# Kernel tuning notes

Hardware: AMD Instinct MI355X
Metric: run time of the kernel (lower is better)

The kernel has to match this reference:

```python
import jax, jax.numpy as jnp
import numpy as np

N = 64        # n_nodes per graph
H = 128       # hidden channels (128x0e + 128x1o)
NB = 8        # radial bessel basis size
L = 2         # num_interactions
R_MAX = 5.0
AVG_NEIGH = 63.0
DIM = 3       # output vector dim
B = 64        # batch (vmapped)
T = 32        # time-embedding dim
S = 5         # num_species


def _edges(n):
    # fully-connected graph, no self loops (static shapes, jit-friendly)
    s, r = np.meshgrid(np.arange(n), np.arange(n), indexing='ij')
    m = s != r
    return jnp.asarray(s[m]), jnp.asarray(r[m])


def setup_inputs() -> dict:
    key = jax.random.key(0)
    ks = jax.random.split(key, 12)
    sc = 0.05
    return {
        'positions': jax.random.normal(ks[0], (B, N, 3), jnp.float32),
        'node_features': jax.random.randint(ks[1], (B, N), 0, S).astype(jnp.int64),
        'global_features': jax.random.normal(ks[2], (B, T), jnp.float32),
        'emb': jax.random.normal(ks[3], (S, H), jnp.float32) * sc,
        'Wt': jax.random.normal(ks[4], (T, H), jnp.float32) * sc,
        'Wr1': jax.random.normal(ks[5], (L, NB, H), jnp.float32) * sc,
        'Wr2': jax.random.normal(ks[6], (L, H, H), jnp.float32) * sc,
        'Wupd': jax.random.normal(ks[7], (L, H, H), jnp.float32) * sc,
        'Wmix': jax.random.normal(ks[8], (L, H, H), jnp.float32) * sc,
        'Wg1': jax.random.normal(ks[9], (H, H), jnp.float32) * sc,
        'Wg2': jax.random.normal(ks[10], (H, H), jnp.float32) * sc,
        'final_scaling': jnp.ones((), jnp.float32),
    }


def _call_single(pos, z, t, emb, Wt, Wr1, Wr2, Wupd, Wmix, Wg1, Wg2, final_scaling):
    snd, rcv = _edges(N)
    ev = pos[rcv] - pos[snd]                               # [E,3] edge vectors (gather)
    r = jnp.sqrt(jnp.sum(ev * ev, axis=-1) + 1e-12)        # [E]
    u = ev / r[:, None]                                    # unit directions
    # Bessel radial basis with cosine cutoff (r_max acts as soft radius graph)
    n = jnp.arange(1, NB + 1, dtype=pos.dtype)
    rb = jnp.sin(n * jnp.pi * r[:, None] / R_MAX) / r[:, None]   # [E,NB]
    fc = 0.5 * (jnp.cos(jnp.pi * r / R_MAX) + 1.0) * (r < R_MAX)
    rb = rb * fc[:, None]
    # node embedding from species + time embedding
    h = emb[z] + t @ Wt                                    # [N,H] scalar features
    v = jnp.zeros((N, H, DIM), pos.dtype)                  # vector (1o) features
    for l in range(L):
        w = jax.nn.silu(rb @ Wr1[l]) @ Wr2[l]              # [E,H] radial weights
        m0 = w * h[snd]                                    # [E,H] scalar messages
        m1 = m0[:, :, None] * u[:, None, :]                # [E,H,3] vector messages
        a0 = jax.ops.segment_sum(m0, rcv, num_segments=N) / AVG_NEIGH
        a1 = jax.ops.segment_sum(m1, rcv, num_segments=N) / AVG_NEIGH
        h = h + a0 @ Wupd[l]
        v = v + jnp.einsum('ngd,gh->nhd', a1, Wmix[l])
    # equivariant readout: scalar gate per channel contracts vector channels
    g = jax.nn.silu(h @ Wg1) @ Wg2                         # [N,H]
    out = jnp.einsum('nhd,nh->nd', v, g)                   # [N,3]
    return out * final_scaling


def reference(positions, node_features, global_features, emb, Wt, Wr1, Wr2, Wupd, Wmix, Wg1, Wg2, final_scaling):
    f = lambda p, z, t: _call_single(p, z, t, emb, Wt, Wr1, Wr2, Wupd, Wmix, Wg1, Wg2, final_scaling)
    return jax.vmap(f)(positions, node_features, global_features)
```

## Files before the change

### kernel.cpp

```cpp
#include <hip/hip_runtime.h>
#include <math.h>

#define NN 64
#define HH 128
#define NBB 8
#define TT 32
#define BB 64
#define NROW (BB * NN)
#define PLANE ((size_t)NROW * HH)
#define WR1OFF (8 * 16384)

typedef __attribute__((ext_vector_type(8))) short short8;
typedef __attribute__((ext_vector_type(4))) float f32x4;
typedef __attribute__((ext_vector_type(2))) unsigned int u32x2;

__device__ __forceinline__ float silu_f(float x) {
  return x * __builtin_amdgcn_rcpf(1.0f + __expf(-x));
}

__device__ __forceinline__ unsigned short bf1(float x) {
  __bf16 h = (__bf16)x;
  return *(unsigned short*)&h;
}
__device__ __forceinline__ unsigned bf2(float lo, float hi) {
  return (unsigned)bf1(lo) | ((unsigned)bf1(hi) << 16);
}

__device__ __forceinline__ void gemm8(
    const unsigned short (*sA)[136], const unsigned short* __restrict__ Bp,
    int w, int nlo, int quad, f32x4 C[2]) {
  const short8 z8 = {0, 0, 0, 0, 0, 0, 0, 0};
  short8 afr[4];
#pragma unroll
  for (int kt = 0; kt < 4; ++kt)
    afr[kt] = (nlo < 8) ? *(const short8*)&sA[nlo][kt * 32 + quad * 8] : z8;
#pragma unroll
  for (int nt = 0; nt < 2; ++nt)
#pragma unroll
    for (int kt = 0; kt < 4; ++kt) {
      short8 bfr = *(const short8*)&Bp[((kt * 128 + w * 32 + nt * 16 + nlo) * 4 + quad) * 8];
      C[nt] = __builtin_amdgcn_mfma_f32_16x16x32_bf16(afr[kt], bfr, C[nt], 0, 0, 0);
    }
}

__global__ __launch_bounds__(256) void k_init(
    const float* __restrict__ emb, const int* __restrict__ z,
    const float* __restrict__ gf, const float* __restrict__ Wt,
    const float* __restrict__ Wr1, const float* __restrict__ Wr2,
    const float* __restrict__ Wupd, const float* __restrict__ Wmix,
    const float* __restrict__ Wg1, const float* __restrict__ Wg2,
    float* __restrict__ h, unsigned short* __restrict__ Wpack) {
  __shared__ float tvec[HH];
  __shared__ int sz[NN];
  int b4 = blockIdx.x, tid = threadIdx.x;
  {
    int p2 = b4 * 256 + tid;
    int p = p2 * 2;
    int m = p >> 14;
    int j = p & 7;
    int q = (p >> 3) & 3;
    int n = (p >> 5) & 127;
    int kt = (p >> 12) & 3;
    int k = kt * 32 + q * 8 + j;
    const float* src;
    int base;
    if (m < 2) { src = Wr2; base = m * 16384; }
    else if (m < 4) { src = Wupd; base = (m - 2) * 16384; }
    else if (m < 6) { src = Wmix; base = (m - 4) * 16384; }
    else if (m == 6) { src = Wg1; base = 0; }
    else { src = Wg2; base = 0; }
    float v0 = src[base + k * 128 + n];
    float v1 = src[base + (k + 1) * 128 + n];
    *(unsigned*)&Wpack[p] = bf2(v0, v1);
  }
  if (tid < 32) {
    int e = b4 * 32 + tid;
    int l = e >> 12, p = e & 4095;
    int n = p >> 5, q = (p >> 3) & 3, j = p & 7;
    float val = (q == 0) ? Wr1[l * NBB * HH + j * HH + n] : 0.f;
    Wpack[WR1OFF + l * 4096 + p] = bf1(val);
  }
  if (b4 < 64) {
    int b = b4;
    if (tid < NN) sz[tid] = z[b * NN + tid];
    if (tid < HH) {
      float acc = 0.f;
#pragma unroll
      for (int k = 0; k < TT; ++k) acc += gf[b * TT + k] * Wt[k * HH + tid];
      tvec[tid] = acc;
    }
    __syncthreads();
    for (int i = tid; i < NN * HH; i += 256) {
      int n = i >> 7, c = i & 127;
      h[(size_t)b * NN * HH + i] = emb[sz[n] * HH + c] + tvec[c];
    }
  }
}

__global__ __launch_bounds__(256) void k_layer0(
    const float* __restrict__ pos, const float* __restrict__ hA,
    unsigned short* __restrict__ apout, const unsigned short* __restrict__ Wpack) {
  __shared__ __align__(16) unsigned short sh_S[NN][136];
  __shared__ __align__(16) unsigned short sh_M0T[4][32][72];
  __shared__ __align__(16) unsigned short sh_rbh[2][NN][8];
  __shared__ __align__(16) unsigned short sh_ub[2][4][NN];

  int blk = blockIdx.x;
  int b = blk >> 4, rp4 = blk & 15;
  int r0 = rp4 * 4;
  int tid = threadIdx.x;
  int w = tid >> 6, lane = tid & 63;
  int nlo = lane & 15, quad = lane >> 4;

  f32x4 hbv[4][2];
#pragma unroll
  for (int mt = 0; mt < 4; ++mt)
#pragma unroll
    for (int nt = 0; nt < 2; ++nt)
#pragma unroll
      for (int reg = 0; reg < 4; ++reg)
        hbv[mt][nt][reg] =
            hA[((size_t)b * NN + mt * 16 + quad * 4 + reg) * HH + w * 32 + nt * 16 + nlo];

  const unsigned short* Wr1p = Wpack + WR1OFF;
  short8 bw[2];
#pragma unroll
  for (int nt = 0; nt < 2; ++nt)
    bw[nt] = *(const short8*)&Wr1p[((w * 32 + nt * 16 + nlo) * 4 + quad) * 8];
  const unsigned short* Bbase = Wpack;
  short8 bfr[4][2];
#pragma unroll
  for (int kt = 0; kt < 4; ++kt)
#pragma unroll
    for (int nt = 0; nt < 2; ++nt)
      bfr[kt][nt] = *(const short8*)&Bbase[((kt * 128 + w * 32 + nt * 16 + nlo) * 4 + quad) * 8];

  const short8 zero8 = {0, 0, 0, 0, 0, 0, 0, 0};

#pragma unroll
  for (int pp = 0; pp < 2; ++pp) {
    int rb0 = r0 + pp * 2;
    {
      int s = tid & 63;
      int ksel = (tid >> 6) & 1;
      int ri = (tid >> 7) & 1;
      int r = rb0 + ri;
      const float* pb = pos + b * NN * 3;
      float dx = pb[r * 3 + 0] - pb[s * 3 + 0];
      float dy = pb[r * 3 + 1] - pb[s * 3 + 1];
      float dz = pb[r * 3 + 2] - pb[s * 3 + 2];
      float rr = sqrtf(dx * dx + dy * dy + dz * dz + 1e-12f);
      float inv = __builtin_amdgcn_rcpf(rr);
      const float invAvg = 1.0f / 63.0f;
      if (ksel == 0) {
        float ia = inv * invAvg;
        sh_ub[ri][1][s] = bf1(dx * ia);
        sh_ub[ri][2][s] = bf1(dy * ia);
        sh_ub[ri][3][s] = bf1(dz * ia);
      } else {
        sh_ub[ri][0][s] = bf1(invAvg);
      }
      const float PI_OVER_5 = 0.628318530717958647692f;
      float fc = (s != r && rr < 5.0f) ? 0.5f * (__cosf(PI_OVER_5 * rr) + 1.0f) : 0.0f;
      float base = PI_OVER_5 * rr;
      float sc = inv * fc;
      int k0 = ksel * 4;
      float v0 = __sinf((float)(k0 + 1) * base) * sc;
      float v1 = __sinf((float)(k0 + 2) * base) * sc;
      float v2 = __sinf((float)(k0 + 3) * base) * sc;
      float v3 = __sinf((float)(k0 + 4) * base) * sc;
      *(unsigned*)&sh_rbh[ri][s][k0]     = bf2(v0, v1);
      *(unsigned*)&sh_rbh[ri][s][k0 + 2] = bf2(v2, v3);
    }
    __syncthreads();

    short8 au[2][2];
#pragma unroll
    for (int ri = 0; ri < 2; ++ri)
#pragma unroll
      for (int kt = 0; kt < 2; ++kt)
        au[ri][kt] = (nlo < 4) ? *(const short8*)&sh_ub[ri][nlo][kt * 32 + quad * 8] : zero8;

#pragma unroll
    for (int ri = 0; ri < 2; ++ri) {
#pragma unroll
      for (int mtp = 0; mtp < 2; ++mtp) {
        f32x4 Cs[2][2];
#pragma unroll
        for (int mi = 0; mi < 2; ++mi)
#pragma unroll
          for (int nt = 0; nt < 2; ++nt) Cs[mi][nt] = (f32x4){0.f, 0.f, 0.f, 0.f};
#pragma unroll
        for (int mi = 0; mi < 2; ++mi) {
          int mt = mtp * 2 + mi;
          short8 afr = (quad == 0) ? *(const short8*)&sh_rbh[ri][mt * 16 + nlo][0] : zero8;
#pragma unroll
          for (int nt = 0; nt < 2; ++nt)
            Cs[mi][nt] = __builtin_amdgcn_mfma_f32_16x16x32_bf16(afr, bw[nt], Cs[mi][nt], 0, 0, 0);
        }
#pragma unroll
        for (int mi = 0; mi < 2; ++mi)
#pragma unroll
          for (int nt = 0; nt < 2; ++nt)
#pragma unroll
            for (int reg = 0; reg < 4; ++reg) {
              int s = (mtp * 2 + mi) * 16 + quad * 4 + reg;
              int c = w * 32 + nt * 16 + nlo;
              sh_S[s][c] = bf1(silu_f(Cs[mi][nt][reg]));
            }
      }
      __syncthreads();

#pragma unroll
      for (int mt = 0; mt < 4; ++mt) {
        short8 afr[4];
        int s_a = mt * 16 + nlo;
#pragma unroll
        for (int kt = 0; kt < 4; ++kt)
          afr[kt] = *(const short8*)&sh_S[s_a][kt * 32 + quad * 8];
#pragma unroll
        for (int nt = 0; nt < 2; ++nt) {
          f32x4 C = {0.f, 0.f, 0.f, 0.f};
#pragma unroll
          for (int kt = 0; kt < 4; ++kt)
            C = __builtin_amdgcn_mfma_f32_16x16x32_bf16(afr[kt], bfr[kt][nt], C, 0, 0, 0);
          f32x4 m0 = C * hbv[mt][nt];
          u32x2 pk;
          pk.x = bf2(m0[0], m0[1]);
          pk.y = bf2(m0[2], m0[3]);
          *(u32x2*)&sh_M0T[w][nt * 16 + nlo][mt * 16 + quad * 4] = pk;
        }
      }
      {
        f32x4 Cu[2] = {{0, 0, 0, 0}, {0, 0, 0, 0}};
#pragma unroll
        for (int nt = 0; nt < 2; ++nt)
#pragma unroll
          for (int kt = 0; kt < 2; ++kt) {
            short8 bm = *(const short8*)&sh_M0T[w][nt * 16 + nlo][kt * 32 + quad * 8];
            Cu[nt] = __builtin_amdgcn_mfma_f32_16x16x32_bf16(au[ri][kt], bm, Cu[nt], 0, 0, 0);
          }
        if (quad == 0) {
#pragma unroll
          for (int nt = 0; nt < 2; ++nt) {
            size_t base = (size_t)(b * NN + rb0 + ri) * HH + w * 32 + nt * 16 + nlo;
#pragma unroll
            for (int reg = 0; reg < 4; ++reg)
              apout[reg * PLANE + base] = bf1(Cu[nt][reg]);
          }
        }
      }
      if (!(pp == 1 && ri == 1)) __syncthreads();
    }
  }
}

__global__ __launch_bounds__(256) void k_fused(
    const float* __restrict__ pos, const float* __restrict__ hA,
    unsigned short* __restrict__ apbf, const unsigned short* __restrict__ Wpack,
    const float* __restrict__ fs, float* __restrict__ out) {
  __shared__ __align__(16) unsigned char smem[38912];
  unsigned short (*sh_S)[136]      = (unsigned short (*)[136])smem;
  unsigned short (*sh_M0T)[32][72] = (unsigned short (*)[32][72])(smem + 17408);
  unsigned short (*sh_rbh)[NN][8]  = (unsigned short (*)[NN][8])(smem + 35840);
  unsigned short (*sh_ub)[4][NN]   = (unsigned short (*)[4][NN])(smem + 37888);

  int blk = blockIdx.x;
  int b = blk >> 3, u8 = blk & 7;
  int tid = threadIdx.x;
  int w = tid >> 6, lane = tid & 63;
  int nlo = lane & 15, quad = lane >> 4;
  const short8 zero8 = {0, 0, 0, 0, 0, 0, 0, 0};

  f32x4 hbv[4][2];
#pragma unroll
  for (int mt = 0; mt < 4; ++mt)
#pragma unroll
    for (int nt = 0; nt < 2; ++nt)
#pragma unroll
      for (int reg = 0; reg < 4; ++reg)
        hbv[mt][nt][reg] =
            hA[((size_t)b * NN + mt * 16 + quad * 4 + reg) * HH + w * 32 + nt * 16 + nlo];

  for (int i = tid; i < NN * 64; i += 256) {
    int s = i >> 6, c2 = (i & 63) * 2;
    *(unsigned*)&sh_S[s][c2] =
        *(const unsigned*)&apbf[((size_t)b * NN + s) * HH + c2];
  }
  __syncthreads();
  {
    const unsigned short* Bu = Wpack + 2 * 16384;
#pragma unroll
    for (int mt = 0; mt < 4; ++mt) {
      short8 afr[4];
#pragma unroll
      for (int kt = 0; kt < 4; ++kt)
        afr[kt] = *(const short8*)&sh_S[mt * 16 + nlo][kt * 32 + quad * 8];
#pragma unroll
      for (int nt = 0; nt < 2; ++nt)
#pragma unroll
        for (int kt = 0; kt < 4; ++kt) {
          short8 bfr2 = *(const short8*)&Bu[((kt * 128 + w * 32 + nt * 16 + nlo) * 4 + quad) * 8];
          hbv[mt][nt] = __builtin_amdgcn_mfma_f32_16x16x32_bf16(afr[kt], bfr2, hbv[mt][nt], 0, 0, 0);
        }
    }
  }
  __syncthreads();

  const unsigned short* Wr1p = Wpack + WR1OFF + 4096;
  short8 bw[2];
#pragma unroll
  for (int nt = 0; nt < 2; ++nt)
    bw[nt] = *(const short8*)&Wr1p[((w * 32 + nt * 16 + nlo) * 4 + quad) * 8];
  const unsigned short* Bbase = Wpack + 16384;
  short8 bfr[4][2];
#pragma unroll
  for (int kt = 0; kt < 4; ++kt)
#pragma unroll
    for (int nt = 0; nt < 2; ++nt)
      bfr[kt][nt] = *(const short8*)&Bbase[((kt * 128 + w * 32 + nt * 16 + nlo) * 4 + quad) * 8];

  for (int unit = 0; unit < 2; ++unit) {
    int r0 = (u8 * 2 + unit) * 4;
#pragma unroll
    for (int pp = 0; pp < 2; ++pp) {
      int rb0 = r0 + pp * 2;
      {
        int s = tid & 63;
        int ksel = (tid >> 6) & 1;
        int ri = (tid >> 7) & 1;
        int r = rb0 + ri;
        const float* pb = pos + b * NN * 3;
        float dx = pb[r * 3 + 0] - pb[s * 3 + 0];
        float dy = pb[r * 3 + 1] - pb[s * 3 + 1];
        float dz = pb[r * 3 + 2] - pb[s * 3 + 2];
        float rr = sqrtf(dx * dx + dy * dy + dz * dz + 1e-12f);
        float inv = __builtin_amdgcn_rcpf(rr);
        const float invAvg = 1.0f / 63.0f;
        if (ksel == 0) {
          float ia = inv * invAvg;
          sh_ub[ri][1][s] = bf1(dx * ia);
          sh_ub[ri][2][s] = bf1(dy * ia);
          sh_ub[ri][3][s] = bf1(dz * ia);
        } else {
          sh_ub[ri][0][s] = bf1(invAvg);
        }
        const float PI_OVER_5 = 0.628318530717958647692f;
        float fc = (s != r && rr < 5.0f) ? 0.5f * (__cosf(PI_OVER_5 * rr) + 1.0f) : 0.0f;
        float base = PI_OVER_5 * rr;
        float sc = inv * fc;
        int k0 = ksel * 4;
        float v0 = __sinf((float)(k0 + 1) * base) * sc;
        float v1 = __sinf((float)(k0 + 2) * base) * sc;
        float v2 = __sinf((float)(k0 + 3) * base) * sc;
        float v3 = __sinf((float)(k0 + 4) * base) * sc;
        *(unsigned*)&sh_rbh[ri][s][k0]     = bf2(v0, v1);
        *(unsigned*)&sh_rbh[ri][s][k0 + 2] = bf2(v2, v3);
      }
      __syncthreads();

      short8 au[2][2];
#pragma unroll
      for (int ri = 0; ri < 2; ++ri)
#pragma unroll
        for (int kt = 0; kt < 2; ++kt)
          au[ri][kt] = (nlo < 4) ? *(const short8*)&sh_ub[ri][nlo][kt * 32 + quad * 8] : zero8;

#pragma unroll
      for (int ri = 0; ri < 2; ++ri) {
#pragma unroll
        for (int mtp = 0; mtp < 2; ++mtp) {
          f32x4 Cs[2][2];
#pragma unroll
          for (int mi = 0; mi < 2; ++mi)
#pragma unroll
            for (int nt = 0; nt < 2; ++nt) Cs[mi][nt] = (f32x4){0.f, 0.f, 0.f, 0.f};
#pragma unroll
          for (int mi = 0; mi < 2; ++mi) {
            int mt = mtp * 2 + mi;
            short8 afr = (quad == 0) ? *(const short8*)&sh_rbh[ri][mt * 16 + nlo][0] : zero8;
#pragma unroll
            for (int nt = 0; nt < 2; ++nt)
              Cs[mi][nt] = __builtin_amdgcn_mfma_f32_16x16x32_bf16(afr, bw[nt], Cs[mi][nt], 0, 0, 0);
          }
#pragma unroll
          for (int mi = 0; mi < 2; ++mi)
#pragma unroll
            for (int nt = 0; nt < 2; ++nt)
#pragma unroll
              for (int reg = 0; reg < 4; ++reg) {
                int s = (mtp * 2 + mi) * 16 + quad * 4 + reg;
                int c = w * 32 + nt * 16 + nlo;
                sh_S[s][c] = bf1(silu_f(Cs[mi][nt][reg]));
              }
        }
        __syncthreads();

#pragma unroll
        for (int mt = 0; mt < 4; ++mt) {
          short8 afr[4];
          int s_a = mt * 16 + nlo;
#pragma unroll
          for (int kt = 0; kt < 4; ++kt)
            afr[kt] = *(const short8*)&sh_S[s_a][kt * 32 + quad * 8];
#pragma unroll
          for (int nt = 0; nt < 2; ++nt) {
            f32x4 C = {0.f, 0.f, 0.f, 0.f};
#pragma unroll
            for (int kt = 0; kt < 4; ++kt)
              C = __builtin_amdgcn_mfma_f32_16x16x32_bf16(afr[kt], bfr[kt][nt], C, 0, 0, 0);
            f32x4 m0 = C * hbv[mt][nt];
            u32x2 pk;
            pk.x = bf2(m0[0], m0[1]);
            pk.y = bf2(m0[2], m0[3]);
            *(u32x2*)&sh_M0T[w][nt * 16 + nlo][mt * 16 + quad * 4] = pk;
          }
        }
        {
          f32x4 Cu[2] = {{0, 0, 0, 0}, {0, 0, 0, 0}};
#pragma unroll
          for (int nt = 0; nt < 2; ++nt)
#pragma unroll
            for (int kt = 0; kt < 2; ++kt) {
              short8 bm = *(const short8*)&sh_M0T[w][nt * 16 + nlo][kt * 32 + quad * 8];
              Cu[nt] = __builtin_amdgcn_mfma_f32_16x16x32_bf16(au[ri][kt], bm, Cu[nt], 0, 0, 0);
            }
          if (quad == 0) {
#pragma unroll
            for (int nt = 0; nt < 2; ++nt) {
              size_t base = (size_t)(b * NN + rb0 + ri) * HH + w * 32 + nt * 16 + nlo;
#pragma unroll
              for (int reg = 0; reg < 4; ++reg)
                apbf[(4 + reg) * PLANE + base] = bf1(Cu[nt][reg]);
            }
          }
        }
        __syncthreads();
      }
    }
  }

  {
    unsigned short (*sh_a)[8][136] = (unsigned short (*)[8][136])smem;
    unsigned short (*sh_h)[136]    = (unsigned short (*)[136])(smem + 17408);
    float (*red)[8][3]             = (float (*)[8][3])(smem + 17408 + 2176);
    int row0 = blk * 8;
    for (int i = tid; i < 8 * 8 * 64; i += 256) {
      int p = i >> 9, rr = (i >> 6) & 7, c2 = (i & 63) * 2;
      *(unsigned*)&sh_a[p][rr][c2] =
          *(const unsigned*)&apbf[p * PLANE + (size_t)(row0 + rr) * HH + c2];
    }
    f32x4 Ch[2];
#pragma unroll
    for (int nt = 0; nt < 2; ++nt)
#pragma unroll
      for (int reg = 0; reg < 4; ++reg)
        Ch[nt][reg] = (quad < 2)
            ? hA[(size_t)(row0 + quad * 4 + reg) * HH + w * 32 + nt * 16 + nlo] : 0.f;
    __syncthreads();
    gemm8(sh_a[0], Wpack + 2 * 16384, w, nlo, quad, Ch);
    gemm8(sh_a[4], Wpack + 3 * 16384, w, nlo, quad, Ch);
    f32x4 Cx[2] = {{0,0,0,0},{0,0,0,0}};
    f32x4 Cy[2] = {{0,0,0,0},{0,0,0,0}};
    f32x4 Cz[2] = {{0,0,0,0},{0,0,0,0}};
    gemm8(sh_a[1], Wpack + 4 * 16384, w, nlo, quad, Cx);
    gemm8(sh_a[5], Wpack + 5 * 16384, w, nlo, quad, Cx);
    gemm8(sh_a[2], Wpack + 4 * 16384, w, nlo, quad, Cy);
    gemm8(sh_a[6], Wpack + 5 * 16384, w, nlo, quad, Cy);
    gemm8(sh_a[3], Wpack + 4 * 16384, w, nlo, quad, Cz);
    gemm8(sh_a[7], Wpack + 5 * 16384, w, nlo, quad, Cz);
    if (quad < 2) {
#pragma unroll
      for (int nt = 0; nt < 2; ++nt)
#pragma unroll
        for (int reg = 0; reg < 4; ++reg)
          sh_h[quad * 4 + reg][w * 32 + nt * 16 + nlo] = bf1(Ch[nt][reg]);
    }
    __syncthreads();
    unsigned short (*sh_q)[136] = sh_a[0];
    f32x4 Cq[2] = {{0,0,0,0},{0,0,0,0}};
    gemm8(sh_h, Wpack + 6 * 16384, w, nlo, quad, Cq);
    if (quad < 2) {
#pragma unroll
      for (int nt = 0; nt < 2; ++nt)
#pragma unroll
        for (int reg = 0; reg < 4; ++reg)
          sh_q[quad * 4 + reg][w * 32 + nt * 16 + nlo] = bf1(silu_f(Cq[nt][reg]));
    }
    __syncthreads();
    f32x4 Cg[2] = {{0,0,0,0},{0,0,0,0}};
    gemm8(sh_q, Wpack + 7 * 16384, w, nlo, quad, Cg);
    float pr[3][4];
#pragma unroll
    for (int d = 0; d < 3; ++d)
#pragma unroll
      for (int reg = 0; reg < 4; ++reg) pr[d][reg] = 0.f;
#pragma unroll
    for (int nt = 0; nt < 2; ++nt)
#pragma unroll
      for (int reg = 0; reg < 4; ++reg) {
        float gv = Cg[nt][reg];
        pr[0][reg] += gv * Cx[nt][reg];
        pr[1][reg] += gv * Cy[nt][reg];
        pr[2][reg] += gv * Cz[nt][reg];
      }
#pragma unroll
    for (int off = 1; off < 16; off <<= 1)
#pragma unroll
      for (int d = 0; d < 3; ++d)
#pragma unroll
        for (int reg = 0; reg < 4; ++reg)
          pr[d][reg] += __shfl_xor(pr[d][reg], off);
    if (nlo == 0 && quad < 2) {
#pragma unroll
      for (int d = 0; d < 3; ++d)
#pragma unroll
        for (int reg = 0; reg < 4; ++reg)
          red[w][quad * 4 + reg][d] = pr[d][reg];
    }
    __syncthreads();
    if (tid < 24) {
      int row = tid / 3, d = tid % 3;
      float s = red[0][row][d] + red[1][row][d] + red[2][row][d] + red[3][row][d];
      out[(size_t)(row0 + row) * 3 + d] = s * fs[0];
    }
  }
}

extern "C" void kernel_launch(void* const* d_in, const int* in_sizes, int n_in,
                              void* d_out, int out_size, void* d_ws, size_t ws_size,
                              hipStream_t stream) {
  const float* pos  = (const float*)d_in[0];
  const int*   z    = (const int*)d_in[1];
  const float* gf   = (const float*)d_in[2];
  const float* emb  = (const float*)d_in[3];
  const float* Wt   = (const float*)d_in[4];
  const float* Wr1  = (const float*)d_in[5];
  const float* Wr2  = (const float*)d_in[6];
  const float* Wupd = (const float*)d_in[7];
  const float* Wmix = (const float*)d_in[8];
  const float* Wg1  = (const float*)d_in[9];
  const float* Wg2  = (const float*)d_in[10];
  const float* fs   = (const float*)d_in[11];
  float* out = (float*)d_out;

  float* ws = (float*)d_ws;
  float* hA = ws;
  unsigned short* apbf = (unsigned short*)(ws + PLANE);
  unsigned short* Wpack = (unsigned short*)(ws + 5 * PLANE);

  k_init<<<dim3(256), dim3(256), 0, stream>>>(emb, z, gf, Wt, Wr1, Wr2, Wupd,
                                              Wmix, Wg1, Wg2, hA, Wpack);
  k_layer0<<<dim3(BB * 16), dim3(256), 0, stream>>>(pos, hA, apbf, Wpack);
  k_fused<<<dim3(512), dim3(256), 0, stream>>>(pos, hA, apbf, Wpack, fs, out);
}
```

Measured before the change: 141.3 us.

## Keep layer-1 aggregates in LDS and compute edge features for four receivers at once

The fused kernel now writes the layer-1 aggregated messages (planes 4-7) directly into a shared-memory buffer that the readout stage reads, instead of storing them to global memory and reading them back. Both layer kernels also compute edge geometry for all four receivers in one pass, which halves the barrier-separated prep phases. This removes a global round trip and some synchronisation. In exchange, LDS use per block grows (about 50 KB in the fused kernel), which may reduce occupancy.

```diff
diff --git a/kernel.cpp b/kernel.cpp
--- a/kernel.cpp
+++ b/kernel.cpp
@@ -102,8 +102,8 @@
     unsigned short* __restrict__ apout, const unsigned short* __restrict__ Wpack) {
   __shared__ __align__(16) unsigned short sh_S[NN][136];
   __shared__ __align__(16) unsigned short sh_M0T[4][32][72];
-  __shared__ __align__(16) unsigned short sh_rbh[2][NN][8];
-  __shared__ __align__(16) unsigned short sh_ub[2][4][NN];
+  __shared__ __align__(16) unsigned short sh_rbh[4][NN][8];
+  __shared__ __align__(16) unsigned short sh_ub[4][4][NN];
 
   int blk = blockIdx.x;
   int b = blk >> 4, rp4 = blk & 15;
@@ -111,6 +111,7 @@
   int tid = threadIdx.x;
   int w = tid >> 6, lane = tid & 63;
   int nlo = lane & 15, quad = lane >> 4;
+  const short8 zero8 = {0, 0, 0, 0, 0, 0, 0, 0};
 
   f32x4 hbv[4][2];
 #pragma unroll
@@ -135,16 +136,188 @@
     for (int nt = 0; nt < 2; ++nt)
       bfr[kt][nt] = *(const short8*)&Bbase[((kt * 128 + w * 32 + nt * 16 + nlo) * 4 + quad) * 8];
 
+  {
+    int s = tid & 63;
+    int ri4 = tid >> 6;
+    int r = r0 + ri4;
+    const float* pb = pos + b * NN * 3;
+    float dx = pb[r * 3 + 0] - pb[s * 3 + 0];
+    float dy = pb[r * 3 + 1] - pb[s * 3 + 1];
+    float dz = pb[r * 3 + 2] - pb[s * 3 + 2];
+    float rr = sqrtf(dx * dx + dy * dy + dz * dz + 1e-12f);
+    float inv = __builtin_amdgcn_rcpf(rr);
+    const float invAvg = 1.0f / 63.0f;
+    float ia = inv * invAvg;
+    sh_ub[ri4][0][s] = bf1(invAvg);
+    sh_ub[ri4][1][s] = bf1(dx * ia);
+    sh_ub[ri4][2][s] = bf1(dy * ia);
+    sh_ub[ri4][3][s] = bf1(dz * ia);
+    const float PI_OVER_5 = 0.628318530717958647692f;
+    float fc = (s != r && rr < 5.0f) ? 0.5f * (__cosf(PI_OVER_5 * rr) + 1.0f) : 0.0f;
+    float base = PI_OVER_5 * rr;
+    float sc = inv * fc;
+#pragma unroll
+    for (int k0 = 0; k0 < 8; k0 += 4) {
+      float v0 = __sinf((float)(k0 + 1) * base) * sc;
+      float v1 = __sinf((float)(k0 + 2) * base) * sc;
+      float v2 = __sinf((float)(k0 + 3) * base) * sc;
+      float v3 = __sinf((float)(k0 + 4) * base) * sc;
+      *(unsigned*)&sh_rbh[ri4][s][k0]     = bf2(v0, v1);
+      *(unsigned*)&sh_rbh[ri4][s][k0 + 2] = bf2(v2, v3);
+    }
+  }
+  __syncthreads();
+
+#pragma unroll
+  for (int rsel = 0; rsel < 4; ++rsel) {
+#pragma unroll
+    for (int mtp = 0; mtp < 2; ++mtp) {
+      f32x4 Cs[2][2];
+#pragma unroll
+      for (int mi = 0; mi < 2; ++mi)
+#pragma unroll
+        for (int nt = 0; nt < 2; ++nt) Cs[mi][nt] = (f32x4){0.f, 0.f, 0.f, 0.f};
+#pragma unroll
+      for (int mi = 0; mi < 2; ++mi) {
+        int mt = mtp * 2 + mi;
+        short8 afr = (quad == 0) ? *(const short8*)&sh_rbh[rsel][mt * 16 + nlo][0] : zero8;
+#pragma unroll
+        for (int nt = 0; nt < 2; ++nt)
+          Cs[mi][nt] = __builtin_amdgcn_mfma_f32_16x16x32_bf16(afr, bw[nt], Cs[mi][nt], 0, 0, 0);
+      }
+#pragma unroll
+      for (int mi = 0; mi < 2; ++mi)
+#pragma unroll
+        for (int nt = 0; nt < 2; ++nt)
+#pragma unroll
+          for (int reg = 0; reg < 4; ++reg) {
+            int s = (mtp * 2 + mi) * 16 + quad * 4 + reg;
+            int c = w * 32 + nt * 16 + nlo;
+            sh_S[s][c] = bf1(silu_f(Cs[mi][nt][reg]));
+          }
+    }
+    __syncthreads();
+
+#pragma unroll
+    for (int mt = 0; mt < 4; ++mt) {
+      short8 afr[4];
+      int s_a = mt * 16 + nlo;
+#pragma unroll
+      for (int kt = 0; kt < 4; ++kt)
+        afr[kt] = *(const short8*)&sh_S[s_a][kt * 32 + quad * 8];
+#pragma unroll
+      for (int nt = 0; nt < 2; ++nt) {
+        f32x4 C = {0.f, 0.f, 0.f, 0.f};
+#pragma unroll
+        for (int kt = 0; kt < 4; ++kt)
+          C = __builtin_amdgcn_mfma_f32_16x16x32_bf16(afr[kt], bfr[kt][nt], C, 0, 0, 0);
+        f32x4 m0 = C * hbv[mt][nt];
+        u32x2 pk;
+        pk.x = bf2(m0[0], m0[1]);
+        pk.y = bf2(m0[2], m0[3]);
+        *(u32x2*)&sh_M0T[w][nt * 16 + nlo][mt * 16 + quad * 4] = pk;
+      }
+    }
+    {
+      short8 au[2];
+#pragma unroll
+      for (int kt = 0; kt < 2; ++kt)
+        au[kt] = (nlo < 4) ? *(const short8*)&sh_ub[rsel][nlo][kt * 32 + quad * 8] : zero8;
+      f32x4 Cu[2] = {{0, 0, 0, 0}, {0, 0, 0, 0}};
+#pragma unroll
+      for (int nt = 0; nt < 2; ++nt)
+#pragma unroll
+        for (int kt = 0; kt < 2; ++kt) {
+          short8 bm = *(const short8*)&sh_M0T[w][nt * 16 + nlo][kt * 32 + quad * 8];
+          Cu[nt] = __builtin_amdgcn_mfma_f32_16x16x32_bf16(au[kt], bm, Cu[nt], 0, 0, 0);
+        }
+      if (quad == 0) {
+#pragma unroll
+        for (int nt = 0; nt < 2; ++nt) {
+          size_t base = (size_t)(b * NN + r0 + rsel) * HH + w * 32 + nt * 16 + nlo;
+#pragma unroll
+          for (int reg = 0; reg < 4; ++reg)
+            apout[reg * PLANE + base] = bf1(Cu[nt][reg]);
+        }
+      }
+    }
+    if (rsel != 3) __syncthreads();
+  }
+}
+
+__global__ __launch_bounds__(256) void k_fused(
+    const float* __restrict__ pos, const float* __restrict__ hA,
+    unsigned short* __restrict__ apbf, const unsigned short* __restrict__ Wpack,
+    const float* __restrict__ fs, float* __restrict__ out) {
+  __shared__ __align__(16) unsigned char smem[50688];
+  unsigned short (*sh_S)[136]      = (unsigned short (*)[136])smem;
+  unsigned short (*sh_M0T)[32][72] = (unsigned short (*)[32][72])(smem + 17408);
+  unsigned short (*sh_rbh)[NN][8]  = (unsigned short (*)[NN][8])(smem + 35840);
+  unsigned short (*sh_ub)[4][NN]   = (unsigned short (*)[4][NN])(smem + 39936);
+  unsigned short (*sh_a47)[8][136] = (unsigned short (*)[8][136])(smem + 41984);
+
+  int blk = blockIdx.x;
+  int b = blk >> 3, u8 = blk & 7;
+  int tid = threadIdx.x;
+  int w = tid >> 6, lane = tid & 63;
+  int nlo = lane & 15, quad = lane >> 4;
   const short8 zero8 = {0, 0, 0, 0, 0, 0, 0, 0};
 
-#pragma unroll
-  for (int pp = 0; pp < 2; ++pp) {
-    int rb0 = r0 + pp * 2;
+  f32x4 hbv[4][2];
+#pragma unroll
+  for (int mt = 0; mt < 4; ++mt)
+#pragma unroll
+    for (int nt = 0; nt < 2; ++nt)
+#pragma unroll
+      for (int reg = 0; reg < 4; ++reg)
+        hbv[mt][nt][reg] =
+            hA[((size_t)b * NN + mt * 16 + quad * 4 + reg) * HH + w * 32 + nt * 16 + nlo];
+
+  for (int i = tid; i < NN * 64; i += 256) {
+    int s = i >> 6, c2 = (i & 63) * 2;
+    *(unsigned*)&sh_S[s][c2] =
+        *(const unsigned*)&apbf[((size_t)b * NN + s) * HH + c2];
+  }
+  __syncthreads();
+  {
+    const unsigned short* Bu = Wpack + 2 * 16384;
+#pragma unroll
+    for (int mt = 0; mt < 4; ++mt) {
+      short8 afr[4];
+#pragma unroll
+      for (int kt = 0; kt < 4; ++kt)
+        afr[kt] = *(const short8*)&sh_S[mt * 16 + nlo][kt * 32 + quad * 8];
+#pragma unroll
+      for (int nt = 0; nt < 2; ++nt)
+#pragma unroll
+        for (int kt = 0; kt < 4; ++kt) {
+          short8 bfr2 = *(const short8*)&Bu[((kt * 128 + w * 32 + nt * 16 + nlo) * 4 + quad) * 8];
+          hbv[mt][nt] = __builtin_amdgcn_mfma_f32_16x16x32_bf16(afr[kt], bfr2, hbv[mt][nt], 0, 0, 0);
+        }
+    }
+  }
+  __syncthreads();
+
+  const unsigned short* Wr1p = Wpack + WR1OFF + 4096;
+  short8 bw[2];
+#pragma unroll
+  for (int nt = 0; nt < 2; ++nt)
+    bw[nt] = *(const short8*)&Wr1p[((w * 32 + nt * 16 + nlo) * 4 + quad) * 8];
+  const unsigned short* Bbase = Wpack + 16384;
+  short8 bfr[4][2];
+#pragma unroll
+  for (int kt = 0; kt < 4; ++kt)
+#pragma unroll
+    for (int nt = 0; nt < 2; ++nt)
+      bfr[kt][nt] = *(const short8*)&Bbase[((kt * 128 + w * 32 + nt * 16 + nlo) * 4 + quad) * 8];
+
+  for (int unit = 0; unit < 2; ++unit) {
+    int r0 = u8 * 8 + unit * 4;
+
     {
       int s = tid & 63;
-      int ksel = (tid >> 6) & 1;
-      int ri = (tid >> 7) & 1;
-      int r = rb0 + ri;
+      int ri4 = tid >> 6;
+      int r = r0 + ri4;
       const float* pb = pos + b * NN * 3;
       float dx = pb[r * 3 + 0] - pb[s * 3 + 0];
       float dy = pb[r * 3 + 1] - pb[s * 3 + 1];
@@ -152,37 +325,30 @@
       float rr = sqrtf(dx * dx + dy * dy + dz * dz + 1e-12f);
       float inv = __builtin_amdgcn_rcpf(rr);
       const float invAvg = 1.0f / 63.0f;
-      if (ksel == 0) {
-        float ia = inv * invAvg;
-        sh_ub[ri][1][s] = bf1(dx * ia);
-        sh_ub[ri][2][s] = bf1(dy * ia);
-        sh_ub[ri][3][s] = bf1(dz * ia);
-      } else {
-        sh_ub[ri][0][s] = bf1(invAvg);
-      }
+      float ia = inv * invAvg;
+      sh_ub[ri4][0][s] = bf1(invAvg);
+      sh_ub[ri4][1][s] = bf1(dx * ia);
+      sh_ub[ri4][2][s] = bf1(dy * ia);
+      sh_ub[ri4][3][s] = bf1(dz * ia);
       const float PI_OVER_5 = 0.628318530717958647692f;
       float fc = (s != r && rr < 5.0f) ? 0.5f * (__cosf(PI_OVER_5 * rr) + 1.0f) : 0.0f;
       float base = PI_OVER_5 * rr;
       float sc = inv * fc;
-      int k0 = ksel * 4;
-      float v0 = __sinf((float)(k0 + 1) * base) * sc;
-      float v1 = __sinf((float)(k0 + 2) * base) * sc;
-      float v2 = __sinf((float)(k0 + 3) * base) * sc;
-      float v3 = __sinf((float)(k0 + 4) * base) * sc;
-      *(unsigned*)&sh_rbh[ri][s][k0]     = bf2(v0, v1);
-      *(unsigned*)&sh_rbh[ri][s][k0 + 2] = bf2(v2, v3);
-    }
-    __syncthreads();
-
-    short8 au[2][2];
-#pragma unroll
-    for (int ri = 0; ri < 2; ++ri)
-#pragma unroll
-      for (int kt = 0; kt < 2; ++kt)
-        au[ri][kt] = (nlo < 4) ? *(const short8*)&sh_ub[ri][nlo][kt * 32 + quad * 8] : zero8;
-
-#pragma unroll
-    for (int ri = 0; ri < 2; ++ri) {
+#pragma unroll
+      for (int k0 = 0; k0 < 8; k0 += 4) {
+        float v0 = __sinf((float)(k0 + 1) * base) * sc;
+        float v1 = __sinf((float)(k0 + 2) * base) * sc;
+        float v2 = __sinf((float)(k0 + 3) * base) * sc;
+        float v3 = __sinf((float)(k0 + 4) * base) * sc;
+        *(unsigned*)&sh_rbh[ri4][s][k0]     = bf2(v0, v1);
+        *(unsigned*)&sh_rbh[ri4][s][k0 + 2] = bf2(v2, v3);
+      }
+    }
+    __syncthreads();
+
+#pragma unroll
+    for (int rsel = 0; rsel < 4; ++rsel) {
+      int lr = unit * 4 + rsel;
 #pragma unroll
       for (int mtp = 0; mtp < 2; ++mtp) {
         f32x4 Cs[2][2];
@@ -193,7 +359,7 @@
 #pragma unroll
         for (int mi = 0; mi < 2; ++mi) {
           int mt = mtp * 2 + mi;
-          short8 afr = (quad == 0) ? *(const short8*)&sh_rbh[ri][mt * 16 + nlo][0] : zero8;
+          short8 afr = (quad == 0) ? *(const short8*)&sh_rbh[rsel][mt * 16 + nlo][0] : zero8;
 #pragma unroll
           for (int nt = 0; nt < 2; ++nt)
             Cs[mi][nt] = __builtin_amdgcn_mfma_f32_16x16x32_bf16(afr, bw[nt], Cs[mi][nt], 0, 0, 0);
@@ -232,222 +398,40 @@
         }
       }
       {
+        short8 au[2];
+#pragma unroll
+        for (int kt = 0; kt < 2; ++kt)
+          au[kt] = (nlo < 4) ? *(const short8*)&sh_ub[rsel][nlo][kt * 32 + quad * 8] : zero8;
         f32x4 Cu[2] = {{0, 0, 0, 0}, {0, 0, 0, 0}};
 #pragma unroll
         for (int nt = 0; nt < 2; ++nt)
 #pragma unroll
           for (int kt = 0; kt < 2; ++kt) {
             short8 bm = *(const short8*)&sh_M0T[w][nt * 16 + nlo][kt * 32 + quad * 8];
-            Cu[nt] = __builtin_amdgcn_mfma_f32_16x16x32_bf16(au[ri][kt], bm, Cu[nt], 0, 0, 0);
+            Cu[nt] = __builtin_amdgcn_mfma_f32_16x16x32_bf16(au[kt], bm, Cu[nt], 0, 0, 0);
           }
         if (quad == 0) {
 #pragma unroll
           for (int nt = 0; nt < 2; ++nt) {
-            size_t base = (size_t)(b * NN + rb0 + ri) * HH + w * 32 + nt * 16 + nlo;
+            int c = w * 32 + nt * 16 + nlo;
 #pragma unroll
             for (int reg = 0; reg < 4; ++reg)
-              apout[reg * PLANE + base] = bf1(Cu[nt][reg]);
+              sh_a47[reg][lr][c] = bf1(Cu[nt][reg]);
           }
         }
       }
-      if (!(pp == 1 && ri == 1)) __syncthreads();
-    }
-  }
-}
-
-__global__ __launch_bounds__(256) void k_fused(
-    const float* __restrict__ pos, const float* __restrict__ hA,
-    unsigned short* __restrict__ apbf, const unsigned short* __restrict__ Wpack,
-    const float* __restrict__ fs, float* __restrict__ out) {
-  __shared__ __align__(16) unsigned char smem[38912];
-  unsigned short (*sh_S)[136]      = (unsigned short (*)[136])smem;
-  unsigned short (*sh_M0T)[32][72] = (unsigned short (*)[32][72])(smem + 17408);
-  unsigned short (*sh_rbh)[NN][8]  = (unsigned short (*)[NN][8])(smem + 35840);
-  unsigned short (*sh_ub)[4][NN]   = (unsigned short (*)[4][NN])(smem + 37888);
-
-  int blk = blockIdx.x;
-  int b = blk >> 3, u8 = blk & 7;
-  int tid = threadIdx.x;
-  int w = tid >> 6, lane = tid & 63;
-  int nlo = lane & 15, quad = lane >> 4;
-  const short8 zero8 = {0, 0, 0, 0, 0, 0, 0, 0};
-
-  f32x4 hbv[4][2];
-#pragma unroll
-  for (int mt = 0; mt < 4; ++mt)
-#pragma unroll
-    for (int nt = 0; nt < 2; ++nt)
-#pragma unroll
-      for (int reg = 0; reg < 4; ++reg)
-        hbv[mt][nt][reg] =
-            hA[((size_t)b * NN + mt * 16 + quad * 4 + reg) * HH + w * 32 + nt * 16 + nlo];
-
-  for (int i = tid; i < NN * 64; i += 256) {
-    int s = i >> 6, c2 = (i & 63) * 2;
-    *(unsigned*)&sh_S[s][c2] =
-        *(const unsigned*)&apbf[((size_t)b * NN + s) * HH + c2];
-  }
-  __syncthreads();
+      __syncthreads();
+    }
+  }
+
   {
-    const unsigned short* Bu = Wpack + 2 * 16384;
-#pragma unroll
-    for (int mt = 0; mt < 4; ++mt) {
-      short8 afr[4];
-#pragma unroll
-      for (int kt = 0; kt < 4; ++kt)
-        afr[kt] = *(const short8*)&sh_S[mt * 16 + nlo][kt * 32 + quad * 8];
-#pragma unroll
-      for (int nt = 0; nt < 2; ++nt)
-#pragma unroll
-        for (int kt = 0; kt < 4; ++kt) {
-          short8 bfr2 = *(const short8*)&Bu[((kt * 128 + w * 32 + nt * 16 + nlo) * 4 + quad) * 8];
-          hbv[mt][nt] = __builtin_amdgcn_mfma_f32_16x16x32_bf16(afr[kt], bfr2, hbv[mt][nt], 0, 0, 0);
-        }
-    }
-  }
-  __syncthreads();
-
-  const unsigned short* Wr1p = Wpack + WR1OFF + 4096;
-  short8 bw[2];
-#pragma unroll
-  for (int nt = 0; nt < 2; ++nt)
-    bw[nt] = *(const short8*)&Wr1p[((w * 32 + nt * 16 + nlo) * 4 + quad) * 8];
-  const unsigned short* Bbase = Wpack + 16384;
-  short8 bfr[4][2];
-#pragma unroll
-  for (int kt = 0; kt < 4; ++kt)
-#pragma unroll
-    for (int nt = 0; nt < 2; ++nt)
-      bfr[kt][nt] = *(const short8*)&Bbase[((kt * 128 + w * 32 + nt * 16 + nlo) * 4 + quad) * 8];
-
-  for (int unit = 0; unit < 2; ++unit) {
-    int r0 = (u8 * 2 + unit) * 4;
-#pragma unroll
-    for (int pp = 0; pp < 2; ++pp) {
-      int rb0 = r0 + pp * 2;
-      {
-        int s = tid & 63;
-        int ksel = (tid >> 6) & 1;
-        int ri = (tid >> 7) & 1;
-        int r = rb0 + ri;
-        const float* pb = pos + b * NN * 3;
-        float dx = pb[r * 3 + 0] - pb[s * 3 + 0];
-        float dy = pb[r * 3 + 1] - pb[s * 3 + 1];
-        float dz = pb[r * 3 + 2] - pb[s * 3 + 2];
-        float rr = sqrtf(dx * dx + dy * dy + dz * dz + 1e-12f);
-        float inv = __builtin_amdgcn_rcpf(rr);
-        const float invAvg = 1.0f / 63.0f;
-        if (ksel == 0) {
-          float ia = inv * invAvg;
-          sh_ub[ri][1][s] = bf1(dx * ia);
-          sh_ub[ri][2][s] = bf1(dy * ia);
-          sh_ub[ri][3][s] = bf1(dz * ia);
-        } else {
-          sh_ub[ri][0][s] = bf1(invAvg);
-        }
-        const float PI_OVER_5 = 0.628318530717958647692f;
-        float fc = (s != r && rr < 5.0f) ? 0.5f * (__cosf(PI_OVER_5 * rr) + 1.0f) : 0.0f;
-        float base = PI_OVER_5 * rr;
-        float sc = inv * fc;
-        int k0 = ksel * 4;
-        float v0 = __sinf((float)(k0 + 1) * base) * sc;
-        float v1 = __sinf((float)(k0 + 2) * base) * sc;
-        float v2 = __sinf((float)(k0 + 3) * base) * sc;
-        float v3 = __sinf((float)(k0 + 4) * base) * sc;
-        *(unsigned*)&sh_rbh[ri][s][k0]     = bf2(v0, v1);
-        *(unsigned*)&sh_rbh[ri][s][k0 + 2] = bf2(v2, v3);
-      }
-      __syncthreads();
-
-      short8 au[2][2];
-#pragma unroll
-      for (int ri = 0; ri < 2; ++ri)
-#pragma unroll
-        for (int kt = 0; kt < 2; ++kt)
-          au[ri][kt] = (nlo < 4) ? *(const short8*)&sh_ub[ri][nlo][kt * 32 + quad * 8] : zero8;
-
-#pragma unroll
-      for (int ri = 0; ri < 2; ++ri) {
-#pragma unroll
-        for (int mtp = 0; mtp < 2; ++mtp) {
-          f32x4 Cs[2][2];
-#pragma unroll
-          for (int mi = 0; mi < 2; ++mi)
-#pragma unroll
-            for (int nt = 0; nt < 2; ++nt) Cs[mi][nt] = (f32x4){0.f, 0.f, 0.f, 0.f};
-#pragma unroll
-          for (int mi = 0; mi < 2; ++mi) {
-            int mt = mtp * 2 + mi;
-            short8 afr = (quad == 0) ? *(const short8*)&sh_rbh[ri][mt * 16 + nlo][0] : zero8;
-#pragma unroll
-            for (int nt = 0; nt < 2; ++nt)
-              Cs[mi][nt] = __builtin_amdgcn_mfma_f32_16x16x32_bf16(afr, bw[nt], Cs[mi][nt], 0, 0, 0);
-          }
-#pragma unroll
-          for (int mi = 0; mi < 2; ++mi)
-#pragma unroll
-            for (int nt = 0; nt < 2; ++nt)
-#pragma unroll
-              for (int reg = 0; reg < 4; ++reg) {
-                int s = (mtp * 2 + mi) * 16 + quad * 4 + reg;
-                int c = w * 32 + nt * 16 + nlo;
-                sh_S[s][c] = bf1(silu_f(Cs[mi][nt][reg]));
-              }
-        }
-        __syncthreads();
-
-#pragma unroll
-        for (int mt = 0; mt < 4; ++mt) {
-          short8 afr[4];
-          int s_a = mt * 16 + nlo;
-#pragma unroll
-          for (int kt = 0; kt < 4; ++kt)
-            afr[kt] = *(const short8*)&sh_S[s_a][kt * 32 + quad * 8];
-#pragma unroll
-          for (int nt = 0; nt < 2; ++nt) {
-            f32x4 C = {0.f, 0.f, 0.f, 0.f};
-#pragma unroll
-            for (int kt = 0; kt < 4; ++kt)
-              C = __builtin_amdgcn_mfma_f32_16x16x32_bf16(afr[kt], bfr[kt][nt], C, 0, 0, 0);
-            f32x4 m0 = C * hbv[mt][nt];
-            u32x2 pk;
-            pk.x = bf2(m0[0], m0[1]);
-            pk.y = bf2(m0[2], m0[3]);
-            *(u32x2*)&sh_M0T[w][nt * 16 + nlo][mt * 16 + quad * 4] = pk;
-          }
-        }
-        {
-          f32x4 Cu[2] = {{0, 0, 0, 0}, {0, 0, 0, 0}};
-#pragma unroll
-          for (int nt = 0; nt < 2; ++nt)
-#pragma unroll
-            for (int kt = 0; kt < 2; ++kt) {
-              short8 bm = *(const short8*)&sh_M0T[w][nt * 16 + nlo][kt * 32 + quad * 8];
-              Cu[nt] = __builtin_amdgcn_mfma_f32_16x16x32_bf16(au[ri][kt], bm, Cu[nt], 0, 0, 0);
-            }
-          if (quad == 0) {
-#pragma unroll
-            for (int nt = 0; nt < 2; ++nt) {
-              size_t base = (size_t)(b * NN + rb0 + ri) * HH + w * 32 + nt * 16 + nlo;
-#pragma unroll
-              for (int reg = 0; reg < 4; ++reg)
-                apbf[(4 + reg) * PLANE + base] = bf1(Cu[nt][reg]);
-            }
-          }
-        }
-        __syncthreads();
-      }
-    }
-  }
-
-  {
-    unsigned short (*sh_a)[8][136] = (unsigned short (*)[8][136])smem;
-    unsigned short (*sh_h)[136]    = (unsigned short (*)[136])(smem + 17408);
-    float (*red)[8][3]             = (float (*)[8][3])(smem + 17408 + 2176);
+    unsigned short (*sh_a03)[8][136] = (unsigned short (*)[8][136])smem;
+    unsigned short (*sh_h)[136]      = (unsigned short (*)[136])(smem + 8704);
+    float (*red)[8][3]               = (float (*)[8][3])(smem + 8704 + 2176);
     int row0 = blk * 8;
-    for (int i = tid; i < 8 * 8 * 64; i += 256) {
+    for (int i = tid; i < 4 * 8 * 64; i += 256) {
       int p = i >> 9, rr = (i >> 6) & 7, c2 = (i & 63) * 2;
-      *(unsigned*)&sh_a[p][rr][c2] =
+      *(unsigned*)&sh_a03[p][rr][c2] =
           *(const unsigned*)&apbf[p * PLANE + (size_t)(row0 + rr) * HH + c2];
     }
     f32x4 Ch[2];
@@ -458,17 +442,17 @@
         Ch[nt][reg] = (quad < 2)
             ? hA[(size_t)(row0 + quad * 4 + reg) * HH + w * 32 + nt * 16 + nlo] : 0.f;
     __syncthreads();
-    gemm8(sh_a[0], Wpack + 2 * 16384, w, nlo, quad, Ch);
-    gemm8(sh_a[4], Wpack + 3 * 16384, w, nlo, quad, Ch);
+    gemm8(sh_a03[0], Wpack + 2 * 16384, w, nlo, quad, Ch);
+    gemm8(sh_a47[0], Wpack + 3 * 16384, w, nlo, quad, Ch);
     f32x4 Cx[2] = {{0,0,0,0},{0,0,0,0}};
     f32x4 Cy[2] = {{0,0,0,0},{0,0,0,0}};
     f32x4 Cz[2] = {{0,0,0,0},{0,0,0,0}};
-    gemm8(sh_a[1], Wpack + 4 * 16384, w, nlo, quad, Cx);
-    gemm8(sh_a[5], Wpack + 5 * 16384, w, nlo, quad, Cx);
-    gemm8(sh_a[2], Wpack + 4 * 16384, w, nlo, quad, Cy);
-    gemm8(sh_a[6], Wpack + 5 * 16384, w, nlo, quad, Cy);
-    gemm8(sh_a[3], Wpack + 4 * 16384, w, nlo, quad, Cz);
-    gemm8(sh_a[7], Wpack + 5 * 16384, w, nlo, quad, Cz);
+    gemm8(sh_a03[1], Wpack + 4 * 16384, w, nlo, quad, Cx);
+    gemm8(sh_a47[1], Wpack + 5 * 16384, w, nlo, quad, Cx);
+    gemm8(sh_a03[2], Wpack + 4 * 16384, w, nlo, quad, Cy);
+    gemm8(sh_a47[2], Wpack + 5 * 16384, w, nlo, quad, Cy);
+    gemm8(sh_a03[3], Wpack + 4 * 16384, w, nlo, quad, Cz);
+    gemm8(sh_a47[3], Wpack + 5 * 16384, w, nlo, quad, Cz);
     if (quad < 2) {
 #pragma unroll
       for (int nt = 0; nt < 2; ++nt)
@@ -477,7 +461,7 @@
           sh_h[quad * 4 + reg][w * 32 + nt * 16 + nlo] = bf1(Ch[nt][reg]);
     }
     __syncthreads();
-    unsigned short (*sh_q)[136] = sh_a[0];
+    unsigned short (*sh_q)[136] = sh_a03[0];
     f32x4 Cq[2] = {{0,0,0,0},{0,0,0,0}};
     gemm8(sh_h, Wpack + 6 * 16384, w, nlo, quad, Cq);
     if (quad < 2) {
```

Result: faster. 138.3 us, median of 2 (-2.1%).
